# Performance work log

Measured on AMD Instinct MI355X. Metric: run time of the kernel, lower is better.

The kernel has to match this reference:

```python
import jax, jax.numpy as jnp
import numpy as np

BS, N, C = 512, 18, 2048
EPS = 1e-12
BN_SCALE = 1.0 / np.sqrt(1.0 + 1e-5)  # eval-mode BN with running_mean=0, running_var=1


def _normalize(v):
    # F.normalize(p=2, dim=2, eps=1e-12)
    n = jnp.linalg.norm(v, axis=2, keepdims=True)
    return v / jnp.maximum(n, EPS)


def _bn_relu(v, gamma, beta):
    # BatchNorm2d in eval mode (running_mean=0, running_var=1) followed by ReLU
    return jax.nn.relu(v * (gamma * BN_SCALE) + beta)


def _safe_sqrt(r):
    # forward-identical to sqrt (r >= 0 here); avoids NaN grad at r == 0 (diagonal)
    pos = r > 0
    return jnp.where(pos, jnp.sqrt(jnp.where(pos, r, 1.0)), 0.0)


def setup_inputs() -> dict:
    key = jax.random.key(0)
    ks = jax.random.split(key, 10)
    s = 0.02
    return {
        "x": jax.random.normal(ks[0], (BS, N, C), jnp.float32),
        "part_coordinate": jax.random.uniform(ks[1], (BS, N, 4), jnp.float32),
        # conv1: C -> 3 (1x1)
        "w1": jax.random.normal(ks[2], (3, C), jnp.float32) * s,
        "b1": jnp.zeros((3,), jnp.float32),
        # conv2: 4 -> C, BN, ReLU, C -> 3
        "w2a": jax.random.normal(ks[3], (C, 4), jnp.float32) * s,
        "b2a": jnp.zeros((C,), jnp.float32),
        "g2": jnp.ones((C,), jnp.float32),
        "be2": jnp.zeros((C,), jnp.float32),
        "w2b": jax.random.normal(ks[4], (3, C), jnp.float32) * s,
        "b2b": jnp.zeros((3,), jnp.float32),
        # conv: C -> C, BN, ReLU
        "wc": jax.random.normal(ks[5], (C, C), jnp.float32) * s,
        "bc": jnp.zeros((C,), jnp.float32),
        "gc": jnp.ones((C,), jnp.float32),
        "bec": jnp.zeros((C,), jnp.float32),
        # conv3: C -> C, BN, ReLU
        "w3": jax.random.normal(ks[6], (C, C), jnp.float32) * s,
        "b3": jnp.zeros((C,), jnp.float32),
        "g3": jnp.ones((C,), jnp.float32),
        "be3": jnp.zeros((C,), jnp.float32),
    }


def reference(x, part_coordinate, w1, b1, w2a, b2a, g2, be2, w2b, b2b,
              wc, bc, gc, bec, w3, b3, g3, be3):
    # z1 = softmax(conv1(x)) over the 3 clusters
    z1 = jax.nn.softmax(jnp.einsum('bnc,kc->bnk', x, w1) + b1, axis=2)  # [B,N,3]

    # distance_list1: cosine affinities of x and z1
    xn = _normalize(x)
    d1_1 = jnp.einsum('bnc,bmc->bnm', xn, xn)       # [B,N,N]
    z1n = _normalize(z1)
    d2_1 = jnp.einsum('bnk,bmk->bnm', z1n, z1n)     # [B,N,N]

    # z2 = softmax(conv2(part_coordinate))
    h = _bn_relu(jnp.einsum('bnf,cf->bnc', part_coordinate, w2a) + b2a, g2, be2)
    z2 = jax.nn.softmax(jnp.einsum('bnc,kc->bnk', h, w2b) + b2b, axis=2)  # [B,N,3]

    # distance_list2: spatial-center distance + cosine affinity of z2
    yc = part_coordinate[..., 0] + jnp.floor(part_coordinate[..., 2] / 2)
    xc = part_coordinate[..., 1] + jnp.floor(part_coordinate[..., 3] / 2)
    dy = (yc[:, None, :] - yc[:, :, None]) ** 2
    dx = (xc[:, None, :] - xc[:, :, None]) ** 2
    d1_2 = 1.0 - 2.0 * _safe_sqrt(dx + dy)          # [B,N,N]
    z2n = _normalize(z2)
    d2_2 = jnp.einsum('bnk,bmk->bnm', z2n, z2n)     # [B,N,N]

    # encode / decode aggregation over 3 cluster nodes
    z = z1 + z2                                      # [B,N,3]
    enc = z / (jnp.sum(z, axis=1, keepdims=True) + EPS)
    dec = z / (jnp.sum(z, axis=2, keepdims=True) + EPS)
    u = jnp.einsum('bnk,bnc->bkc', enc, x)           # [B,3,C]
    u = _bn_relu(jnp.einsum('bkc,dc->bkd', u, wc) + bc, gc, bec)
    y = jnp.einsum('bnk,bkc->bnc', dec, u)           # [B,N,C]
    y = _bn_relu(jnp.einsum('bnc,dc->bnd', y, w3) + b3, g3, be3) + x

    return (y, d2_1, d1_1, d2_2, d1_2)
```

## Files before the change

### kernel.cpp

```cpp
#include <hip/hip_runtime.h>

#define BS   512
#define NPTS 18
#define CH   2048
#define EPSF 1e-12f
#define BNS  0.9999950000374997f

typedef unsigned short ushort_t;
typedef __attribute__((ext_vector_type(8)))  short bfrag;
typedef __attribute__((ext_vector_type(4)))  float f32x4v;
typedef __attribute__((ext_vector_type(16))) float f32x16;

__device__ inline ushort_t bf16_rne(float f) {
  union { float f; unsigned int u; } c; c.f = f;
  unsigned int u = c.u;
  u += 0x7fffu + ((u >> 16) & 1u);
  return (ushort_t)(u >> 16);
}
__device__ inline float bf16_to_f(ushort_t s) {
  union { float f; unsigned int u; } c; c.u = ((unsigned int)s) << 16;
  return c.f;
}
__device__ inline bfrag cvt8(float4 a, float4 b) {
  bfrag r;
  r[0]=(short)bf16_rne(a.x); r[1]=(short)bf16_rne(a.y);
  r[2]=(short)bf16_rne(a.z); r[3]=(short)bf16_rne(a.w);
  r[4]=(short)bf16_rne(b.x); r[5]=(short)bf16_rne(b.y);
  r[6]=(short)bf16_rne(b.z); r[7]=(short)bf16_rne(b.w);
  return r;
}

__global__ __launch_bounds__(1024, 8) void k_mega(
    const float* __restrict__ x, const float* __restrict__ pc,
    const float* __restrict__ w1, const float* __restrict__ b1,
    const float* __restrict__ w2a, const float* __restrict__ b2a,
    const float* __restrict__ g2, const float* __restrict__ be2,
    const float* __restrict__ w2b, const float* __restrict__ b2b,
    const float* __restrict__ wc, const float* __restrict__ w3,
    ushort_t* __restrict__ wc_bf, ushort_t* __restrict__ w3_bf,
    float* __restrict__ d21, float* __restrict__ d11,
    float* __restrict__ d22, float* __restrict__ d12,
    ushort_t* __restrict__ u_pre, float* __restrict__ dec_out)
{
  const int blk = blockIdx.x, tid = threadIdx.x;

  if (blk >= BS) {
    const int cb = blk - BS;
    const int n4 = CH*CH/4;
    #pragma unroll
    for (int k = 0; k < 4; k++) {
      int gid = cb*4096 + k*1024 + tid;
      const float* src; ushort_t* dst; int i;
      if (gid < n4) { src = wc; dst = wc_bf; i = gid; }
      else          { src = w3; dst = w3_bf; i = gid - n4; }
      float4 v = ((const float4*)src)[i];
      ushort4 o;
      o.x = bf16_rne(v.x); o.y = bf16_rne(v.y);
      o.z = bf16_rne(v.z); o.w = bf16_rne(v.w);
      ((ushort4*)dst)[i] = o;
    }
    return;
  }

  __shared__ __align__(16) ushort_t IMG[18*CH];
  __shared__ __align__(16) float F[2048];
  float* Gt     = F;
  float* l2part = F + 1512;
  float* l2s    = F + 1620;
  float* z1s    = F + 1674;
  float* z2s    = F + 1728;
  float* encs   = F + 1782;
  float* ycs    = F + 1836;
  float* xcs    = F + 1854;
  float* n1inv  = F + 1872;
  float* n2inv  = F + 1890;
  float* rinvS  = F + 1908;
  float* colinv = F + 1926;

  const int b = blk, lane = tid & 63, wv = tid >> 6;

  {
    const float4* x4 = (const float4*)x + (size_t)b*9216;
    #pragma unroll
    for (int k = 0; k < 4; k++) {
      int p = k*1024 + tid;
      float4 a = x4[2*p], c = x4[2*p + 1];
      int row = p >> 8;
      *(bfrag*)((char*)IMG + ((p*16) ^ ((row & 7) << 4))) = cvt8(a, c);
    }
    if (tid < 512) {
      int p = 4096 + tid;
      float4 a = x4[2*p], c = x4[2*p + 1];
      int row = p >> 8;
      *(bfrag*)((char*)IMG + ((p*16) ^ ((row & 7) << 4))) = cvt8(a, c);
    }
  }
  __syncthreads();

  if (wv < 4) {
    const int rc = lane & 31, kh = lane >> 5;
    const int arow = (rc < NPTS) ? rc : (NPTS-1);
    const int amsk = (arow & 7) << 4;
    const int abase = arow*4096;
    const bool isw = (rc >= NPTS) && (rc < NPTS+3);
    const int wrow = isw ? (rc - NPTS) : 0;
    const float* wp = w1 + (size_t)wrow*CH + wv*512 + kh*8;
    f32x16 acc = {0.f,0.f,0.f,0.f,0.f,0.f,0.f,0.f,0.f,0.f,0.f,0.f,0.f,0.f,0.f,0.f};
    #pragma unroll 4
    for (int j = 0; j < 32; j++) {
      const int kb = (wv*512 + j*16 + kh*8)*2;
      bfrag av = *(const bfrag*)((const char*)IMG + ((abase + kb) ^ amsk));
      bfrag bv = av;
      if (isw) bv = cvt8(*(const float4*)(wp + j*16), *(const float4*)(wp + j*16 + 4));
      acc = __builtin_amdgcn_mfma_f32_32x32x16_bf16(av, bv, acc, 0, 0, 0);
    }
    #pragma unroll
    for (int r = 0; r < 16; r++) {
      int orow = (r & 3) + 8*(r >> 2) + 4*kh;
      if (orow < NPTS && rc < 21) Gt[wv*378 + orow*21 + rc] = acc[r];
    }
  } else {
    const int zid = wv - 4, g = zid >> 1, th = zid & 1;
    const float* pcb = pc + (size_t)b*NPTS*4 + g*12;
    float pq[3][4];
    #pragma unroll
    for (int j = 0; j < 3; j++) {
      pq[j][0] = pcb[j*4+0]; pq[j][1] = pcb[j*4+1];
      pq[j][2] = pcb[j*4+2]; pq[j][3] = pcb[j*4+3];
    }
    float acc[3][3];
    #pragma unroll
    for (int j = 0; j < 3; j++) { acc[j][0]=0.f; acc[j][1]=0.f; acc[j][2]=0.f; }
    #pragma unroll 2
    for (int it = 0; it < 16; it++) {
      int c = th*1024 + it*64 + lane;
      const float4 wa = *(const float4*)(w2a + (size_t)c*4);
      float bb = b2a[c], gg = g2[c]*BNS, be = be2[c];
      float wb0 = w2b[c], wb1 = w2b[CH+c], wb2 = w2b[2*CH+c];
      #pragma unroll
      for (int j = 0; j < 3; j++) {
        float v = fmaf(pq[j][3], wa.w, fmaf(pq[j][2], wa.z,
                  fmaf(pq[j][1], wa.y, fmaf(pq[j][0], wa.x, bb))));
        float h = fmaxf(fmaf(v, gg, be), 0.f);
        acc[j][0] = fmaf(h, wb0, acc[j][0]);
        acc[j][1] = fmaf(h, wb1, acc[j][1]);
        acc[j][2] = fmaf(h, wb2, acc[j][2]);
      }
    }
    #pragma unroll
    for (int j = 0; j < 3; j++)
      #pragma unroll
      for (int k = 0; k < 3; k++) {
        float v = acc[j][k];
        #pragma unroll
        for (int off = 32; off; off >>= 1) v += __shfl_xor(v, off);
        if (lane == 0) l2part[zid*9 + j*3 + k] = v;
      }
  }
  __syncthreads();

  if (tid < 378) {
    F[tid] = (F[tid] + F[378+tid]) + (F[756+tid] + F[1134+tid]);
  } else if (tid < 432) {
    int t = tid - 378;
    int p = t/3, k = t - 3*p, g = p/3, pp = p - 3*g;
    l2s[t] = l2part[(g*2)*9 + pp*3+k] + l2part[(g*2+1)*9 + pp*3+k] + b2b[k];
  } else if (tid >= 448 && tid < 466) {
    int n = tid - 448;
    const float* p = pc + (size_t)b*NPTS*4 + n*4;
    ycs[n] = p[0] + floorf(p[2]*0.5f);
    xcs[n] = p[1] + floorf(p[3]*0.5f);
  }
  __syncthreads();
  float* sGl = F;

  if (tid < NPTS) {
    int n = tid;
    float a0 = sGl[n*21+18] + b1[0], a1 = sGl[n*21+19] + b1[1], a2 = sGl[n*21+20] + b1[2];
    float mx = fmaxf(a0, fmaxf(a1, a2));
    float e0 = expf(a0-mx), e1 = expf(a1-mx), e2 = expf(a2-mx);
    float inv = 1.f/(e0+e1+e2);
    float z10 = e0*inv, z11 = e1*inv, z12 = e2*inv;
    z1s[n*3+0]=z10; z1s[n*3+1]=z11; z1s[n*3+2]=z12;
    n1inv[n] = 1.f/fmaxf(sqrtf(z10*z10+z11*z11+z12*z12), EPSF);

    float c0 = l2s[n*3+0], c1 = l2s[n*3+1], c2 = l2s[n*3+2];
    mx = fmaxf(c0, fmaxf(c1, c2));
    e0 = expf(c0-mx); e1 = expf(c1-mx); e2 = expf(c2-mx);
    inv = 1.f/(e0+e1+e2);
    float z20 = e0*inv, z21 = e1*inv, z22 = e2*inv;
    z2s[n*3+0]=z20; z2s[n*3+1]=z21; z2s[n*3+2]=z22;
    n2inv[n] = 1.f/fmaxf(sqrtf(z20*z20+z21*z21+z22*z22), EPSF);

    float zr0 = z10+z20, zr1 = z11+z21, zr2 = z12+z22;
    float rinvv = 1.f/((zr0+zr1+zr2) + EPSF);
    dec_out[(size_t)b*54 + n*3 + 0] = zr0*rinvv;
    dec_out[(size_t)b*54 + n*3 + 1] = zr1*rinvv;
    dec_out[(size_t)b*54 + n*3 + 2] = zr2*rinvv;

    rinvS[n] = 1.f/fmaxf(sqrtf(sGl[n*21+n]), EPSF);
  }
  __syncthreads();

  if (tid < 3) {
    float s = 0.f;
    #pragma unroll
    for (int n = 0; n < NPTS; n++) s += z1s[n*3+tid] + z2s[n*3+tid];
    colinv[tid] = 1.f/(s + EPSF);
  }
  if (tid < NPTS*NPTS) {
    int t = tid;
    int n = t/NPTS, mm = t - n*NPTS;
    float dd21 = (z1s[n*3]*z1s[mm*3] + z1s[n*3+1]*z1s[mm*3+1] + z1s[n*3+2]*z1s[mm*3+2])
                 * n1inv[n]*n1inv[mm];
    float dd22 = (z2s[n*3]*z2s[mm*3] + z2s[n*3+1]*z2s[mm*3+1] + z2s[n*3+2]*z2s[mm*3+2])
                 * n2inv[n]*n2inv[mm];
    float dd11 = sGl[n*21+mm] * rinvS[n]*rinvS[mm];
    float dyv = ycs[mm]-ycs[n], dxv = xcs[mm]-xcs[n];
    float r = dxv*dxv + dyv*dyv;
    float dd12 = 1.f - 2.f*((r > 0.f) ? sqrtf(r) : 0.f);
    size_t o = (size_t)b*NPTS*NPTS + t;
    d21[o] = dd21; d11[o] = dd11; d22[o] = dd22; d12[o] = dd12;
  }
  __syncthreads();
  if (tid < 54) encs[tid] = (z1s[tid]+z2s[tid])*colinv[tid%3];
  __syncthreads();

  {
    const int c0 = tid*2;
    float a0=0.f,a1=0.f,a2=0.f, q0=0.f,q1=0.f,q2=0.f;
    #pragma unroll
    for (int n = 0; n < NPTS; n++) {
      unsigned v = *(const unsigned*)((const char*)IMG + ((n*4096 + c0*2) ^ ((n & 7) << 4)));
      float x0 = bf16_to_f((ushort_t)(v & 0xffff));
      float x1 = bf16_to_f((ushort_t)(v >> 16));
      float e0 = encs[n*3+0], e1 = encs[n*3+1], e2 = encs[n*3+2];
      a0 = fmaf(e0, x0, a0); q0 = fmaf(e0, x1, q0);
      a1 = fmaf(e1, x0, a1); q1 = fmaf(e1, x1, q1);
      a2 = fmaf(e2, x0, a2); q2 = fmaf(e2, x1, q2);
    }
    ushort2 o0, o1, o2;
    o0.x = bf16_rne(a0); o0.y = bf16_rne(q0);
    o1.x = bf16_rne(a1); o1.y = bf16_rne(q1);
    o2.x = bf16_rne(a2); o2.y = bf16_rne(q2);
    *(ushort2*)(u_pre + ((size_t)b*3 + 0)*CH + c0) = o0;
    *(ushort2*)(u_pre + ((size_t)b*3 + 1)*CH + c0) = o1;
    *(ushort2*)(u_pre + ((size_t)b*3 + 2)*CH + c0) = o2;
  }
}

#define GM 1536
#define GK 2048
#define GN 2048

#define STAGE(buf, k0) { \
    _Pragma("unroll") \
    for (int i = 0; i < 4; i++) \
      __builtin_amdgcn_global_load_lds( \
          (const __attribute__((address_space(1))) void*)(Ag + (size_t)(i*32 + ldrow)*GK + (k0)), \
          (__attribute__((address_space(3))) void*)(&Asm[buf][i*2048 + wv*512]), 16, 0, 0); \
    _Pragma("unroll") \
    for (int i = 0; i < 2; i++) \
      __builtin_amdgcn_global_load_lds( \
          (const __attribute__((address_space(1))) void*)(Bg + (size_t)(i*32 + ldrow)*GK + (k0)), \
          (__attribute__((address_space(3))) void*)(&Bsm[buf][i*2048 + wv*512]), 16, 0, 0); }

template<int MODE>
__global__ __launch_bounds__(256) void gemm_mfma(
    const ushort_t* __restrict__ A, const ushort_t* __restrict__ B,
    void* __restrict__ Cout, const float* __restrict__ bias,
    const float* __restrict__ gamma, const float* __restrict__ beta)
{
  __shared__ ushort_t Asm[2][128*64];
  __shared__ ushort_t Bsm[2][64*64];
  const int tid  = threadIdx.x;
  const int lane = tid & 63, wv = tid >> 6;
  const int mb = blockIdx.x % (GM/128), nb = blockIdx.x / (GM/128);
  const int wr = (wv >> 1) * 64, wc = (wv & 1) * 32;

  f32x4v acc[4][2];
  #pragma unroll
  for (int m = 0; m < 4; m++)
    #pragma unroll
    for (int n = 0; n < 2; n++)
      acc[m][n] = (f32x4v){0.f, 0.f, 0.f, 0.f};

  const int ldrow = tid >> 3;
  const int ldcol = (((tid & 7) ^ (ldrow & 7)) * 8);
  const ushort_t* Ag = A + (size_t)(mb*128)*GK + ldcol;
  const ushort_t* Bg = B + (size_t)(nb*64)*GK + ldcol;
  const int r15 = lane & 15, khi = lane >> 4;

  STAGE(0, 0)
  __syncthreads();
  for (int t = 0; t < GK/64; ++t) {
    const int cur = t & 1;
    if (t < GK/64 - 1) STAGE(cur ^ 1, (t+1)*64)
    #pragma unroll
    for (int ks = 0; ks < 2; ks++) {
      bfrag af[4], bfv[2];
      #pragma unroll
      for (int m = 0; m < 4; m++) {
        const int ar = wr + m*16 + r15;
        af[m] = *(const bfrag*)(&Asm[cur][ar*64 + ((ks*32 + khi*8) ^ ((ar & 7)*8))]);
      }
      #pragma unroll
      for (int n = 0; n < 2; n++) {
        const int br = wc + n*16 + r15;
        bfv[n] = *(const bfrag*)(&Bsm[cur][br*64 + ((ks*32 + khi*8) ^ ((br & 7)*8))]);
      }
      #pragma unroll
      for (int m = 0; m < 4; m++)
        #pragma unroll
        for (int n = 0; n < 2; n++)
          acc[m][n] = __builtin_amdgcn_mfma_f32_16x16x32_bf16(
              af[m], bfv[n], acc[m][n], 0, 0, 0);
    }
    __syncthreads();
  }

  #pragma unroll
  for (int n = 0; n < 2; n++) {
    const int gc = nb*64 + wc + n*16 + r15;
    float bi = 0.f, ga = 0.f, be = 0.f;
    if (MODE == 1) { bi = bias[gc]; ga = gamma[gc]*BNS; be = beta[gc]; }
    #pragma unroll
    for (int m = 0; m < 4; m++) {
      const int gr0 = mb*128 + wr + m*16 + khi*4;
      #pragma unroll
      for (int r = 0; r < 4; r++) {
        float v = acc[m][n][r];
        if (MODE == 1) {
          v = fmaxf(fmaf(v + bi, ga, be), 0.f);
          ((ushort_t*)Cout)[(size_t)(gr0 + r)*GN + gc] = bf16_rne(v);
        } else {
          ((float*)Cout)[(size_t)(gr0 + r)*GN + gc] = v;
        }
      }
    }
  }
}

__global__ __launch_bounds__(256) void k_epi(
    const float* __restrict__ x, const float* __restrict__ V,
    const float* __restrict__ dec, const float* __restrict__ b3,
    const float* __restrict__ g3, const float* __restrict__ be3,
    float* __restrict__ y)
{
  __shared__ float4 lv[3*512];
  __shared__ float4 lmul[512], ladd[512];
  __shared__ float ld[54];
  const int b = blockIdx.x, tid = threadIdx.x;

  const float4* v4 = (const float4*)(V + (size_t)b*3*CH);
  for (int i = tid; i < 1536; i += 256) lv[i] = v4[i];
  const float4* g34  = (const float4*)g3;
  const float4* b34  = (const float4*)b3;
  const float4* be34 = (const float4*)be3;
  for (int i = tid; i < 512; i += 256) {
    float4 g = g34[i], bb = b34[i], be = be34[i];
    float4 mu, ad;
    mu.x = g.x*BNS; mu.y = g.y*BNS; mu.z = g.z*BNS; mu.w = g.w*BNS;
    ad.x = fmaf(bb.x, mu.x, be.x); ad.y = fmaf(bb.y, mu.y, be.y);
    ad.z = fmaf(bb.z, mu.z, be.z); ad.w = fmaf(bb.w, mu.w, be.w);
    lmul[i] = mu; ladd[i] = ad;
  }
  if (tid < 54) ld[tid] = dec[(size_t)b*54 + tid];
  __syncthreads();

  for (int r = 0; r < NPTS; r++) {
    float d0 = ld[r*3+0], d1 = ld[r*3+1], d2 = ld[r*3+2];
    const float4* xr = (const float4*)(x + ((size_t)b*NPTS + r)*CH);
    float4* yr = (float4*)(y + ((size_t)b*NPTS + r)*CH);
    for (int i = tid; i < 512; i += 256) {
      float4 v0 = lv[i], v1 = lv[512+i], v2 = lv[1024+i];
      float4 mu = lmul[i], ad = ladd[i], xa = xr[i];
      float4 o;
      o.x = fmaxf(fmaf(fmaf(d0,v0.x, fmaf(d1,v1.x, d2*v2.x)), mu.x, ad.x), 0.f) + xa.x;
      o.y = fmaxf(fmaf(fmaf(d0,v0.y, fmaf(d1,v1.y, d2*v2.y)), mu.y, ad.y), 0.f) + xa.y;
      o.z = fmaxf(fmaf(fmaf(d0,v0.z, fmaf(d1,v1.z, d2*v2.z)), mu.z, ad.z), 0.f) + xa.z;
      o.w = fmaxf(fmaf(fmaf(d0,v0.w, fmaf(d1,v1.w, d2*v2.w)), mu.w, ad.w), 0.f) + xa.w;
      yr[i] = o;
    }
  }
}

extern "C" void kernel_launch(void* const* d_in, const int* in_sizes, int n_in,
                              void* d_out, int out_size, void* d_ws, size_t ws_size,
                              hipStream_t stream) {
  const float* x   = (const float*)d_in[0];
  const float* pc  = (const float*)d_in[1];
  const float* w1  = (const float*)d_in[2];
  const float* b1  = (const float*)d_in[3];
  const float* w2a = (const float*)d_in[4];
  const float* b2a = (const float*)d_in[5];
  const float* g2  = (const float*)d_in[6];
  const float* be2 = (const float*)d_in[7];
  const float* w2b = (const float*)d_in[8];
  const float* b2b = (const float*)d_in[9];
  const float* wc  = (const float*)d_in[10];
  const float* bc  = (const float*)d_in[11];
  const float* gc  = (const float*)d_in[12];
  const float* bec = (const float*)d_in[13];
  const float* w3  = (const float*)d_in[14];
  const float* b3  = (const float*)d_in[15];
  const float* g3  = (const float*)d_in[16];
  const float* be3 = (const float*)d_in[17];

  float* out = (float*)d_out;
  float* y   = out;
  float* d21 = out + (size_t)BS*NPTS*CH;
  float* d11 = d21 + (size_t)BS*NPTS*NPTS;
  float* d22 = d11 + (size_t)BS*NPTS*NPTS;
  float* d12 = d22 + (size_t)BS*NPTS*NPTS;

  char* ybytes = (char*)y;
  ushort_t* u_pre_bf = (ushort_t*)(ybytes + 0);
  ushort_t* u_bf     = (ushort_t*)(ybytes + 6291456);
  ushort_t* wc_bf    = (ushort_t*)(ybytes + 12582912);
  ushort_t* w3_bf    = (ushort_t*)(ybytes + 20971520);

  float* V    = (float*)d_ws;
  float* decb = V + (size_t)BS*3*CH;

  k_mega<<<BS + 512, 1024, 0, stream>>>(x, pc, w1, b1, w2a, b2a, g2, be2,
                                        w2b, b2b, wc, w3, wc_bf, w3_bf,
                                        d21, d11, d22, d12, u_pre_bf, decb);
  gemm_mfma<1><<<(GM/128)*(GN/64), 256, 0, stream>>>(u_pre_bf, wc_bf, u_bf, bc, gc, bec);
  gemm_mfma<0><<<(GM/128)*(GN/64), 256, 0, stream>>>(u_bf, w3_bf, V, nullptr, nullptr, nullptr);
  k_epi<<<BS, 256, 0, stream>>>(x, V, decb, b3, g3, be3, y);
}
```

Baseline: 145.3 us.

## Fuse second GEMM with output epilogue and move scratch buffers to workspace

Merges the second MFMA GEMM (u @ w3) with the per-point decode/BN/ReLU/residual epilogue. Each block now computes a 96x64 tile in 96-row-by-64-column chunks, keeps V in LDS as bf16, and writes y directly. This removes the fp32 V round trip through global memory and one kernel launch. Because y is now written by the fused kernel while other blocks still read GEMM inputs, u_bf and w3_bf move from the y region to the workspace. The risks are extra bf16 rounding of V, fewer blocks (512), and narrower 32-byte x/y accesses per thread, which may coalesce less well.

```diff
diff --git a/kernel.cpp b/kernel.cpp
--- a/kernel.cpp
+++ b/kernel.cpp
@@ -265,10 +265,9 @@
           (const __attribute__((address_space(1))) void*)(Bg + (size_t)(i*32 + ldrow)*GK + (k0)), \
           (__attribute__((address_space(3))) void*)(&Bsm[buf][i*2048 + wv*512]), 16, 0, 0); }
 
-template<int MODE>
-__global__ __launch_bounds__(256) void gemm_mfma(
+__global__ __launch_bounds__(256) void gemm1(
     const ushort_t* __restrict__ A, const ushort_t* __restrict__ B,
-    void* __restrict__ Cout, const float* __restrict__ bias,
+    ushort_t* __restrict__ Cout, const float* __restrict__ bias,
     const float* __restrict__ gamma, const float* __restrict__ beta)
 {
   __shared__ ushort_t Asm[2][128*64];
@@ -322,65 +321,144 @@
   #pragma unroll
   for (int n = 0; n < 2; n++) {
     const int gc = nb*64 + wc + n*16 + r15;
-    float bi = 0.f, ga = 0.f, be = 0.f;
-    if (MODE == 1) { bi = bias[gc]; ga = gamma[gc]*BNS; be = beta[gc]; }
+    float bi = bias[gc], ga = gamma[gc]*BNS, be = beta[gc];
     #pragma unroll
     for (int m = 0; m < 4; m++) {
       const int gr0 = mb*128 + wr + m*16 + khi*4;
       #pragma unroll
       for (int r = 0; r < 4; r++) {
-        float v = acc[m][n][r];
-        if (MODE == 1) {
-          v = fmaxf(fmaf(v + bi, ga, be), 0.f);
-          ((ushort_t*)Cout)[(size_t)(gr0 + r)*GN + gc] = bf16_rne(v);
-        } else {
-          ((float*)Cout)[(size_t)(gr0 + r)*GN + gc] = v;
+        float v = fmaxf(fmaf(acc[m][n][r] + bi, ga, be), 0.f);
+        Cout[(size_t)(gr0 + r)*GN + gc] = bf16_rne(v);
+      }
+    }
+  }
+}
+
+#define STAGE2(buf, k0) { \
+    _Pragma("unroll") \
+    for (int i = 0; i < 3; i++) { \
+      int u = i*256 + tid; \
+      int arw = u >> 3, ac8 = u & 7; \
+      __builtin_amdgcn_global_load_lds( \
+          (const __attribute__((address_space(1))) void*)(Au + (size_t)(mb*96 + arw)*GK + (k0) + ((ac8 ^ (arw & 7))*8)), \
+          (__attribute__((address_space(3))) void*)(&A2[buf][u*8]), 16, 0, 0); \
+    } \
+    _Pragma("unroll") \
+    for (int i = 0; i < 2; i++) { \
+      int u = i*256 + tid; \
+      int brw = u >> 3, bc8 = u & 7; \
+      __builtin_amdgcn_global_load_lds( \
+          (const __attribute__((address_space(1))) void*)(Bw + (size_t)(nb*64 + brw)*GK + (k0) + ((bc8 ^ (brw & 7))*8)), \
+          (__attribute__((address_space(3))) void*)(&B2[buf][u*8]), 16, 0, 0); \
+    } }
+
+__global__ __launch_bounds__(256) void gemm_epi(
+    const ushort_t* __restrict__ Au, const ushort_t* __restrict__ Bw,
+    const float* __restrict__ x, const float* __restrict__ dec,
+    const float* __restrict__ b3, const float* __restrict__ g3,
+    const float* __restrict__ be3, float* __restrict__ y)
+{
+  __shared__ ushort_t A2[2][96*64];
+  __shared__ ushort_t B2[2][64*64];
+  __shared__ ushort_t Vl[96*68];
+  __shared__ float decl[32*54];
+  __shared__ float mul_[64], add_[64];
+  const int tid = threadIdx.x, lane = tid & 63, wv = tid >> 6;
+  const int wg = (blockIdx.x & 7)*64 + (blockIdx.x >> 3);
+  const int mb = wg & 15, nb = wg >> 4;
+  const int wr = (wv >> 1)*48, wc = (wv & 1)*32;
+  const int r15 = lane & 15, khi = lane >> 4;
+
+  for (int i = tid; i < 32*54; i += 256) decl[i] = dec[(size_t)mb*1728 + i];
+  if (tid < 64) {
+    float mu = g3[nb*64 + tid]*BNS;
+    mul_[tid] = mu;
+    add_[tid] = fmaf(b3[nb*64 + tid], mu, be3[nb*64 + tid]);
+  }
+
+  f32x4v acc[3][2];
+  #pragma unroll
+  for (int m = 0; m < 3; m++)
+    #pragma unroll
+    for (int n = 0; n < 2; n++)
+      acc[m][n] = (f32x4v){0.f, 0.f, 0.f, 0.f};
+
+  STAGE2(0, 0)
+  __syncthreads();
+  for (int t = 0; t < GK/64; ++t) {
+    const int cur = t & 1;
+    if (t < GK/64 - 1) STAGE2(cur ^ 1, (t+1)*64)
+    #pragma unroll
+    for (int ks = 0; ks < 2; ks++) {
+      bfrag af[3], bfv[2];
+      #pragma unroll
+      for (int m = 0; m < 3; m++) {
+        const int ar = wr + m*16 + r15;
+        af[m] = *(const bfrag*)(&A2[cur][ar*64 + ((ks*32 + khi*8) ^ ((ar & 7)*8))]);
+      }
+      #pragma unroll
+      for (int n = 0; n < 2; n++) {
+        const int br = wc + n*16 + r15;
+        bfv[n] = *(const bfrag*)(&B2[cur][br*64 + ((ks*32 + khi*8) ^ ((br & 7)*8))]);
+      }
+      #pragma unroll
+      for (int m = 0; m < 3; m++)
+        #pragma unroll
+        for (int n = 0; n < 2; n++)
+          acc[m][n] = __builtin_amdgcn_mfma_f32_16x16x32_bf16(
+              af[m], bfv[n], acc[m][n], 0, 0, 0);
+    }
+    __syncthreads();
+  }
+
+  #pragma unroll
+  for (int n = 0; n < 2; n++) {
+    const int gcl = wc + n*16 + r15;
+    #pragma unroll
+    for (int m = 0; m < 3; m++) {
+      const int gr0 = wr + m*16 + khi*4;
+      #pragma unroll
+      for (int r = 0; r < 4; r++)
+        Vl[(gr0 + r)*68 + gcl] = bf16_rne(acc[m][n][r]);
+    }
+  }
+  __syncthreads();
+
+  {
+    const int bb = tid >> 3, cg = tid & 7;
+    float vr[3][8], mu[8], ad[8];
+    #pragma unroll
+    for (int k = 0; k < 3; k++) {
+      ushort4 v0 = *(const ushort4*)(&Vl[(bb*3 + k)*68 + cg*8]);
+      ushort4 v1 = *(const ushort4*)(&Vl[(bb*3 + k)*68 + cg*8 + 4]);
+      vr[k][0]=bf16_to_f(v0.x); vr[k][1]=bf16_to_f(v0.y);
+      vr[k][2]=bf16_to_f(v0.z); vr[k][3]=bf16_to_f(v0.w);
+      vr[k][4]=bf16_to_f(v1.x); vr[k][5]=bf16_to_f(v1.y);
+      vr[k][6]=bf16_to_f(v1.z); vr[k][7]=bf16_to_f(v1.w);
+    }
+    #pragma unroll
+    for (int j = 0; j < 8; j++) { mu[j] = mul_[cg*8+j]; ad[j] = add_[cg*8+j]; }
+
+    const size_t rowbase = ((size_t)(mb*32 + bb)*NPTS)*CH + nb*64 + cg*8;
+    for (int n = 0; n < NPTS; n++) {
+      float d0 = decl[bb*54 + n*3 + 0];
+      float d1 = decl[bb*54 + n*3 + 1];
+      float d2 = decl[bb*54 + n*3 + 2];
+      const float* xr = x + rowbase + (size_t)n*CH;
+      float* yr = y + rowbase + (size_t)n*CH;
+      #pragma unroll
+      for (int cc = 0; cc < 2; cc++) {
+        float4 xv = *(const float4*)(xr + cc*4);
+        float4 o;
+        #pragma unroll
+        for (int j = 0; j < 4; j++) {
+          int c = cc*4 + j;
+          float val = fmaf(d0, vr[0][c], fmaf(d1, vr[1][c], d2*vr[2][c]));
+          float res = fmaxf(fmaf(val, mu[c], ad[c]), 0.f);
+          ((float*)&o)[j] = res + ((const float*)&xv)[j];
         }
-      }
-    }
-  }
-}
-
-__global__ __launch_bounds__(256) void k_epi(
-    const float* __restrict__ x, const float* __restrict__ V,
-    const float* __restrict__ dec, const float* __restrict__ b3,
-    const float* __restrict__ g3, const float* __restrict__ be3,
-    float* __restrict__ y)
-{
-  __shared__ float4 lv[3*512];
-  __shared__ float4 lmul[512], ladd[512];
-  __shared__ float ld[54];
-  const int b = blockIdx.x, tid = threadIdx.x;
-
-  const float4* v4 = (const float4*)(V + (size_t)b*3*CH);
-  for (int i = tid; i < 1536; i += 256) lv[i] = v4[i];
-  const float4* g34  = (const float4*)g3;
-  const float4* b34  = (const float4*)b3;
-  const float4* be34 = (const float4*)be3;
-  for (int i = tid; i < 512; i += 256) {
-    float4 g = g34[i], bb = b34[i], be = be34[i];
-    float4 mu, ad;
-    mu.x = g.x*BNS; mu.y = g.y*BNS; mu.z = g.z*BNS; mu.w = g.w*BNS;
-    ad.x = fmaf(bb.x, mu.x, be.x); ad.y = fmaf(bb.y, mu.y, be.y);
-    ad.z = fmaf(bb.z, mu.z, be.z); ad.w = fmaf(bb.w, mu.w, be.w);
-    lmul[i] = mu; ladd[i] = ad;
-  }
-  if (tid < 54) ld[tid] = dec[(size_t)b*54 + tid];
-  __syncthreads();
-
-  for (int r = 0; r < NPTS; r++) {
-    float d0 = ld[r*3+0], d1 = ld[r*3+1], d2 = ld[r*3+2];
-    const float4* xr = (const float4*)(x + ((size_t)b*NPTS + r)*CH);
-    float4* yr = (float4*)(y + ((size_t)b*NPTS + r)*CH);
-    for (int i = tid; i < 512; i += 256) {
-      float4 v0 = lv[i], v1 = lv[512+i], v2 = lv[1024+i];
-      float4 mu = lmul[i], ad = ladd[i], xa = xr[i];
-      float4 o;
-      o.x = fmaxf(fmaf(fmaf(d0,v0.x, fmaf(d1,v1.x, d2*v2.x)), mu.x, ad.x), 0.f) + xa.x;
-      o.y = fmaxf(fmaf(fmaf(d0,v0.y, fmaf(d1,v1.y, d2*v2.y)), mu.y, ad.y), 0.f) + xa.y;
-      o.z = fmaxf(fmaf(fmaf(d0,v0.z, fmaf(d1,v1.z, d2*v2.z)), mu.z, ad.z), 0.f) + xa.z;
-      o.w = fmaxf(fmaf(fmaf(d0,v0.w, fmaf(d1,v1.w, d2*v2.w)), mu.w, ad.w), 0.f) + xa.w;
-      yr[i] = o;
+        *(float4*)(yr + cc*4) = o;
+      }
     }
   }
 }
@@ -416,17 +494,15 @@
 
   char* ybytes = (char*)y;
   ushort_t* u_pre_bf = (ushort_t*)(ybytes + 0);
-  ushort_t* u_bf     = (ushort_t*)(ybytes + 6291456);
-  ushort_t* wc_bf    = (ushort_t*)(ybytes + 12582912);
-  ushort_t* w3_bf    = (ushort_t*)(ybytes + 20971520);
-
-  float* V    = (float*)d_ws;
-  float* decb = V + (size_t)BS*3*CH;
+  ushort_t* wc_bf    = (ushort_t*)(ybytes + 6291456);
+
+  ushort_t* u_bf  = (ushort_t*)d_ws;
+  ushort_t* w3_bf = (ushort_t*)((char*)d_ws + 6291456);
+  float*    decb  = (float*)((char*)d_ws + 14680064);
 
   k_mega<<<BS + 512, 1024, 0, stream>>>(x, pc, w1, b1, w2a, b2a, g2, be2,
                                         w2b, b2b, wc, w3, wc_bf, w3_bf,
                                         d21, d11, d22, d12, u_pre_bf, decb);
-  gemm_mfma<1><<<(GM/128)*(GN/64), 256, 0, stream>>>(u_pre_bf, wc_bf, u_bf, bc, gc, bec);
-  gemm_mfma<0><<<(GM/128)*(GN/64), 256, 0, stream>>>(u_bf, w3_bf, V, nullptr, nullptr, nullptr);
-  k_epi<<<BS, 256, 0, stream>>>(x, V, decb, b3, g3, be3, y);
-}
+  gemm1<<<(GM/128)*(GN/64), 256, 0, stream>>>(u_pre_bf, wc_bf, u_bf, bc, gc, bec);
+  gemm_epi<<<512, 256, 0, stream>>>(u_bf, w3_bf, x, decb, b3, g3, be3, y);
+}
```

Result: faster. 131.7 us (-9.3%).
